# Kernel tuning notes

Hardware: AMD Instinct MI355X
Metric: run time of the kernel (lower is better)

Reference implementation:

```python
import jax, jax.numpy as jnp
import numpy as np

N = 50000
E = 1600000
IN_C = 64
HID = 16
HEADS = 4
OUT_C = 1
ATT_SLOPE = 0.2   # GATConv negative_slope for attention logits
ACT_SLOPE = 0.01  # F.leaky_relu default between layers


def _glorot(key, shape):
    fan_in, fan_out = shape[0], shape[-1]
    lim = jnp.sqrt(6.0 / (fan_in + fan_out))
    return jax.random.uniform(key, shape, jnp.float32, -lim, lim)


def setup_inputs() -> dict:
    key = jax.random.key(0)
    ks = jax.random.split(key, 12)
    x = jax.random.normal(ks[0], (N, IN_C), jnp.float32)
    edge_index = jax.random.randint(ks[1], (2, E), 0, N, jnp.int64)
    return {
        "x": x,
        "edge_index": edge_index,
        # GAT layer 1: in -> HID per head, HEADS heads (concat)
        "W1": _glorot(ks[2], (IN_C, HEADS * HID)),
        "att_src1": _glorot(ks[3], (HEADS, HID)),
        "att_dst1": _glorot(ks[4], (HEADS, HID)),
        "b1": jnp.zeros((HEADS * HID,), jnp.float32),
        # GAT layer 2: HEADS*HID -> HID, 1 head
        "W2": _glorot(ks[5], (HEADS * HID, HID)),
        "att_src2": _glorot(ks[6], (1, HID)),
        "att_dst2": _glorot(ks[7], (1, HID)),
        "b2": jnp.zeros((HID,), jnp.float32),
        # final linear
        "Wo": _glorot(ks[8], (HID, OUT_C)),
        "bo": jnp.zeros((OUT_C,), jnp.float32),
    }


def _gat_layer(x, src, dst, W, a_src, a_dst, b, n_nodes):
    """PyG GATConv (eval mode): h = xW; edge logits from additive attention;
    segment softmax over incoming edges of each dst; weighted scatter-sum."""
    H, C = a_src.shape
    h = (x @ W).reshape(n_nodes, H, C)                       # [N, H, C]
    alpha_s = jnp.einsum("nhc,hc->nh", h, a_src)             # [N, H]
    alpha_d = jnp.einsum("nhc,hc->nh", h, a_dst)             # [N, H]
    e = jax.nn.leaky_relu(alpha_s[src] + alpha_d[dst], ATT_SLOPE)  # [E, H]
    m = jax.ops.segment_max(e, dst, num_segments=n_nodes)    # [N, H]
    w = jnp.exp(e - m[dst])
    denom = jax.ops.segment_sum(w, dst, num_segments=n_nodes)
    alpha = w / denom[dst]                                   # [E, H] (self-loops => denom>0)
    out = jax.ops.segment_sum(h[src] * alpha[:, :, None], dst, num_segments=n_nodes)
    return out.reshape(n_nodes, H * C) + b                   # concat heads + bias


def reference(x, edge_index, W1, att_src1, att_dst1, b1,
              W2, att_src2, att_dst2, b2, Wo, bo):
    n = x.shape[0]
    loops = jnp.arange(n, dtype=edge_index.dtype)
    src = jnp.concatenate([edge_index[0], loops])            # add_self_loops=True
    dst = jnp.concatenate([edge_index[1], loops])
    h = _gat_layer(x, src, dst, W1, att_src1, att_dst1, b1, n)
    h = jax.nn.leaky_relu(h, ACT_SLOPE)
    h = _gat_layer(h, src, dst, W2, att_src2, att_dst2, b2, n)
    h = jax.nn.leaky_relu(h, ACT_SLOPE)
    return h @ Wo + bo                                       # [N, 1]
```

## Files before the change

### kernel.cpp

```cpp
#include <hip/hip_runtime.h>
#include <hip/hip_bf16.h>
#include <cstdint>

#define N_NODES 50000
#define N_EDGES 1600000
#define EE (N_EDGES + N_NODES)
#define BSH 7
#define BSIZE 128
#define NBUCKET ((N_NODES + BSIZE - 1) >> BSH)
#define CSH 13
#define CAP 8192
#define GEMM_BLOCKS 3125
#define BIN_BLOCKS 256

__device__ __forceinline__ float lrelu(float x, float s) { return x >= 0.f ? x : s * x; }
__device__ __forceinline__ float bflo(uint32_t v) { return __uint_as_float(v << 16); }
__device__ __forceinline__ float bfhi(uint32_t v) { return __uint_as_float(v & 0xFFFF0000u); }
__device__ __forceinline__ uint32_t bfpackhi(float a) {
    uint32_t u = __float_as_uint(a);
    u += 0x7FFF + ((u >> 16) & 1);
    return u & 0xFFFF0000u;
}
__device__ __forceinline__ uint32_t packbf(float a, float b) {
    uint32_t ua = __float_as_uint(a), ub = __float_as_uint(b);
    ua += 0x7FFF + ((ua >> 16) & 1);
    ub += 0x7FFF + ((ub >> 16) & 1);
    return (ua >> 16) | (ub & 0xFFFF0000u);
}
__device__ __forceinline__ float rdlane(float v, int l) {
    return __uint_as_float(__builtin_amdgcn_readlane(__float_as_uint(v), l));
}

__global__ __launch_bounds__(256) void k_pre(
    const float* __restrict__ x, const float* __restrict__ W1,
    const float* __restrict__ as_w, const float* __restrict__ ad_w,
    uint32_t* __restrict__ h1b, float* __restrict__ as1, float* __restrict__ ad1,
    const int* __restrict__ src, const int* __restrict__ dst,
    int* __restrict__ bcur, uint32_t* __restrict__ binned) {
    if (blockIdx.x < GEMM_BLOCKS) {
        int c = threadIdx.x & 63;
        int wv = threadIdx.x >> 6;
        float wreg[64];
#pragma unroll
        for (int k = 0; k < 64; k++) wreg[k] = W1[k * 64 + c];
        float aw = as_w[c];
        float dw = ad_w[c];
        int base = blockIdx.x * 16 + wv * 4;
#pragma unroll
        for (int r = 0; r < 4; r++) {
            int n = base + r;
            float xr = x[n * 64 + c];
            float a0 = 0.f, a1 = 0.f, a2 = 0.f, a3 = 0.f;
#pragma unroll
            for (int k = 0; k < 64; k += 4) {
                a0 = fmaf(rdlane(xr, k),     wreg[k],     a0);
                a1 = fmaf(rdlane(xr, k + 1), wreg[k + 1], a1);
                a2 = fmaf(rdlane(xr, k + 2), wreg[k + 2], a2);
                a3 = fmaf(rdlane(xr, k + 3), wreg[k + 3], a3);
            }
            float acc = (a0 + a1) + (a2 + a3);
            float other = __shfl_xor(acc, 1, 64);
            if (!(c & 1)) h1b[n * 32 + (c >> 1)] = packbf(acc, other);
            float asv = acc * aw;
            float adv = acc * dw;
#pragma unroll
            for (int off = 1; off < 16; off <<= 1) {
                asv += __shfl_xor(asv, off, 64);
                adv += __shfl_xor(adv, off, 64);
            }
            if ((c & 15) == 0) { as1[n * 4 + (c >> 4)] = asv; ad1[n * 4 + (c >> 4)] = adv; }
        }
        return;
    }
    __shared__ int lcnt[NBUCKET];
    __shared__ int lbase[NBUCKET];
    int bid = blockIdx.x - GEMM_BLOCKS;
    const int T = 16;
    const int CHUNK = 256 * T;
    int nchunks = (EE + CHUNK - 1) / CHUNK;
    for (int ch = bid; ch < nchunks; ch += BIN_BLOCKS) {
        for (int i = threadIdx.x; i < NBUCKET; i += 256) lcnt[i] = 0;
        __syncthreads();
        uint32_t pv[T];
        uint32_t pm[T];
        int base = ch * CHUNK;
#pragma unroll
        for (int k = 0; k < T; k++) {
            int e = base + k * 256 + threadIdx.x;
            if (e < EE) {
                int s, d;
                if (e < N_EDGES) { s = src[e]; d = dst[e]; } else { s = e - N_EDGES; d = s; }
                int b = d >> BSH;
                int r = atomicAdd(&lcnt[b], 1);
                pv[k] = (uint32_t)s | ((uint32_t)(d & (BSIZE - 1)) << 16);
                pm[k] = (uint32_t)r | ((uint32_t)b << 16);
            }
        }
        __syncthreads();
        for (int i = threadIdx.x; i < NBUCKET; i += 256) {
            int c = lcnt[i];
            if (c) lbase[i] = atomicAdd(&bcur[i], c);
        }
        __syncthreads();
#pragma unroll
        for (int k = 0; k < T; k++) {
            int e = base + k * 256 + threadIdx.x;
            if (e < EE) {
                int b = pm[k] >> 16, r = pm[k] & 0xFFFF;
                binned[((size_t)b << CSH) + lbase[b] + r] = pv[k];
            }
        }
        __syncthreads();
    }
}

__global__ __launch_bounds__(512) void kB_sort(const int* __restrict__ bcur, const uint32_t* __restrict__ binned,
                                               const float* __restrict__ as1, const float* __restrict__ ad1,
                                               int* __restrict__ rowdesc, uint32_t* __restrict__ sbn,
                                               uint32_t* __restrict__ wbuf) {
    int b = blockIdx.x, tid = threadIdx.x;
    int p0 = b << CSH;
    int L = bcur[b];
    __shared__ int ncnt[BSIZE];
    __shared__ int sh[BSIZE];
    __shared__ int ncur[BSIZE];
    if (tid < BSIZE) ncnt[tid] = 0;
    __syncthreads();
    for (int i = tid; i < L; i += 512) {
        uint32_t v = binned[p0 + i];
        atomicAdd(&ncnt[(v >> 16) & (BSIZE - 1)], 1);
    }
    __syncthreads();
    int v0 = 0;
    if (tid < BSIZE) { v0 = ncnt[tid]; sh[tid] = v0; }
    __syncthreads();
    for (int off = 1; off < BSIZE; off <<= 1) {
        int t = 0;
        if (tid < BSIZE && tid >= off) t = sh[tid - off];
        __syncthreads();
        if (tid < BSIZE && tid >= off) sh[tid] += t;
        __syncthreads();
    }
    if (tid < BSIZE) {
        int excl = sh[tid] - v0;
        int node = (b << BSH) + tid;
        if (node < N_NODES) rowdesc[node] = excl | (v0 << 13);
        ncur[tid] = excl;
    }
    __syncthreads();
    for (int i = tid; i < L; i += 512) {
        uint32_t v = binned[p0 + i];
        int dl = (v >> 16) & (BSIZE - 1);
        int s = (int)(v & 0xFFFF);
        int pos = atomicAdd(&ncur[dl], 1);
        int node = (b << BSH) + dl;
        float4 a = *(const float4*)(as1 + s * 4);
        float4 d = *(const float4*)(ad1 + node * 4);
        float e0 = a.x + d.x, e1 = a.y + d.y, e2 = a.z + d.z, e3 = a.w + d.w;
        float w0 = __expf(e0 >= 0.f ? e0 : 0.2f * e0);
        float w1 = __expf(e1 >= 0.f ? e1 : 0.2f * e1);
        float w2 = __expf(e2 >= 0.f ? e2 : 0.2f * e2);
        float w3 = __expf(e3 >= 0.f ? e3 : 0.2f * e3);
        sbn[p0 + pos] = (uint32_t)s | ((uint32_t)dl << 16);
        wbuf[(size_t)(p0 + pos) * 2]     = packbf(w0, w1);
        wbuf[(size_t)(p0 + pos) * 2 + 1] = packbf(w2, w3);
    }
}

__global__ __launch_bounds__(256) void k_aggr1f(
    const int* __restrict__ rowdesc, const uint32_t* __restrict__ sbn,
    const uint32_t* __restrict__ wbuf, const uint32_t* __restrict__ h1b,
    const float* __restrict__ b1, const float* __restrict__ W2,
    const float* __restrict__ as2w, const float* __restrict__ ad2w,
    float* __restrict__ h2, float* __restrict__ as2, float* __restrict__ ad2) {
    int n = blockIdx.x * 4 + (threadIdx.x >> 6);
    int lane = threadIdx.x & 63;
    int md = rowdesc[n];
    int begin = ((n >> BSH) << CSH) + (md & (CAP - 1));
    int deg = md >> 13;

    int q = lane >> 4, cl = lane & 15;
    int hc = cl >> 2;
    int wsel = hc >> 1, whalf = hc & 1;

    const uint2* h1b2 = (const uint2*)h1b;
    float acc0 = 0.f, acc1 = 0.f, acc2 = 0.f, acc3 = 0.f, dsum = 0.f;

    int iters = (deg + 3) >> 2;
#pragma unroll 4
    for (int it = 0; it < iters; it++) {
        int idx = it * 4 + q;
        uint32_t sv = sbn[begin + idx];
        uint32_t wp = wbuf[(size_t)(begin + idx) * 2 + wsel];
        float w = whalf ? bfhi(wp) : bflo(wp);
        w = (idx < deg) ? w : 0.f;
        int s = (int)(sv & 0xFFFF);
        uint2 v = h1b2[s * 16 + cl];
        dsum += w;
        acc0 += w * bflo(v.x);
        acc1 += w * bfhi(v.x);
        acc2 += w * bflo(v.y);
        acc3 += w * bfhi(v.y);
    }
#pragma unroll
    for (int off = 16; off <= 32; off <<= 1) {
        acc0 += __shfl_xor(acc0, off, 64);
        acc1 += __shfl_xor(acc1, off, 64);
        acc2 += __shfl_xor(acc2, off, 64);
        acc3 += __shfl_xor(acc3, off, 64);
        dsum += __shfl_xor(dsum, off, 64);
    }
    float dinv = 1.f / dsum;

    float4 bb = *(const float4*)(b1 + 4 * cl);
    float act0 = lrelu(acc0 * dinv + bb.x, 0.01f);
    float act1 = lrelu(acc1 * dinv + bb.y, 0.01f);
    float act2 = lrelu(acc2 * dinv + bb.z, 0.01f);
    float act3 = lrelu(acc3 * dinv + bb.w, 0.01f);

    float g = 0.f;
#pragma unroll
    for (int jj = 0; jj < 4; jj++) {
        int srcl = 4 * q + jj;
        float a0 = __shfl(act0, srcl, 64);
        float a1 = __shfl(act1, srcl, 64);
        float a2 = __shfl(act2, srcl, 64);
        float a3 = __shfl(act3, srcl, 64);
        const float* w2r = W2 + (16 * q + 4 * jj) * 16 + cl;
        g = fmaf(a0, w2r[0],  g);
        g = fmaf(a1, w2r[16], g);
        g = fmaf(a2, w2r[32], g);
        g = fmaf(a3, w2r[48], g);
    }
    g += __shfl_xor(g, 16, 64);
    g += __shfl_xor(g, 32, 64);
    if (lane < 16) h2[n * 16 + cl] = g;
    float asv = g * as2w[cl];
    float adv2 = g * ad2w[cl];
#pragma unroll
    for (int off = 1; off < 16; off <<= 1) {
        asv += __shfl_xor(asv, off, 64);
        adv2 += __shfl_xor(adv2, off, 64);
    }
    if (lane == 0) { as2[n] = asv; ad2[n] = adv2; }
}

__global__ __launch_bounds__(256) void k_w2(
    const int* __restrict__ bcur, const uint32_t* __restrict__ sbn,
    const float* __restrict__ as2, const float* __restrict__ ad2,
    uint32_t* __restrict__ earr2) {
    int slot = blockIdx.x * 256 + threadIdx.x;
    int b = slot >> CSH, i = slot & (CAP - 1);
    if (i >= bcur[b]) return;
    uint32_t v = sbn[slot];
    int s = (int)(v & 0xFFFF);
    int node = (b << BSH) + (int)(v >> 16);
    float e = as2[s] + ad2[node];
    float w = __expf(e >= 0.f ? e : 0.2f * e);
    earr2[slot] = bfpackhi(w) | (uint32_t)s;
}

__global__ __launch_bounds__(256) void k_aggr2(
    const int* __restrict__ rowdesc, const uint32_t* __restrict__ earr2,
    const float* __restrict__ h2,
    const float* __restrict__ b2, const float* __restrict__ Wo,
    const float* __restrict__ bo, float* __restrict__ out) {
    int n = blockIdx.x * 4 + (threadIdx.x >> 6);
    int lane = threadIdx.x & 63;
    int md = rowdesc[n];
    int begin = ((n >> BSH) << CSH) + (md & (CAP - 1));
    int deg = md >> 13;

    int q = lane >> 4, cl = lane & 15;
    const uint32_t* ep = earr2 + begin + q;
    float acc = 0.f, dsum = 0.f;

    int iters = (deg + 3) >> 2;
#pragma unroll 4
    for (int it = 0; it < iters; it++) {
        int idx = it * 4 + q;
        uint32_t ewd = ep[it * 4];
        float w = __uint_as_float(ewd & 0xFFFF0000u);
        w = (idx < deg) ? w : 0.f;
        int s = (int)(ewd & 0xFFFF);
        acc += w * h2[s * 16 + cl];
        dsum += w;
    }
    acc += __shfl_xor(acc, 16, 64);
    acc += __shfl_xor(acc, 32, 64);
    dsum += __shfl_xor(dsum, 16, 64);
    dsum += __shfl_xor(dsum, 32, 64);

    float val = acc / dsum + b2[cl];
    float y = lrelu(val, 0.01f) * Wo[cl];
#pragma unroll
    for (int off = 1; off < 16; off <<= 1) y += __shfl_xor(y, off, 64);
    if (lane == 0) out[n] = y + bo[0];
}

extern "C" void kernel_launch(void* const* d_in, const int* in_sizes, int n_in,
                              void* d_out, int out_size, void* d_ws, size_t ws_size,
                              hipStream_t stream) {
    const float* x    = (const float*)d_in[0];
    const int*   ei   = (const int*)d_in[1];
    const float* W1   = (const float*)d_in[2];
    const float* as1w = (const float*)d_in[3];
    const float* ad1w = (const float*)d_in[4];
    const float* b1   = (const float*)d_in[5];
    const float* W2   = (const float*)d_in[6];
    const float* as2w = (const float*)d_in[7];
    const float* ad2w = (const float*)d_in[8];
    const float* b2   = (const float*)d_in[9];
    const float* Wo   = (const float*)d_in[10];
    const float* bo   = (const float*)d_in[11];
    float* out = (float*)d_out;

    const int* srcp = ei;
    const int* dstp = ei + N_EDGES;

    char* p = (char*)d_ws;
    auto alloc = [&](size_t bytes) -> char* {
        char* r = p;
        p += (bytes + 255) / 256 * 256;
        return r;
    };
    int*      bcur    = (int*)alloc((size_t)(NBUCKET + 1) * 4);
    int*      rowdesc = (int*)alloc((size_t)N_NODES * 4);
    uint32_t* binned  = (uint32_t*)alloc((size_t)NBUCKET * CAP * 4);
    uint32_t* sbn     = (uint32_t*)alloc((size_t)NBUCKET * CAP * 4 + 256);
    uint32_t* wbuf    = (uint32_t*)alloc((size_t)NBUCKET * CAP * 8 + 256);
    uint32_t* earr2   = (uint32_t*)alloc((size_t)NBUCKET * CAP * 4 + 256);
    float*    h2      = (float*)alloc((size_t)N_NODES * 16 * 4);
    uint32_t* h1b     = (uint32_t*)alloc((size_t)N_NODES * 32 * 4);
    float*    as1     = (float*)alloc((size_t)N_NODES * 4 * 4);
    float*    ad1     = (float*)alloc((size_t)N_NODES * 4 * 4);
    float*    as2     = (float*)alloc((size_t)N_NODES * 4);
    float*    ad2     = (float*)alloc((size_t)N_NODES * 4);
    (void)alloc(2 * 1024 * 1024);

    hipMemsetAsync(bcur, 0, (size_t)(NBUCKET + 1) * 4, stream);

    k_pre<<<GEMM_BLOCKS + BIN_BLOCKS, 256, 0, stream>>>(x, W1, as1w, ad1w, h1b, as1, ad1,
                                                        srcp, dstp, bcur, binned);
    kB_sort<<<NBUCKET, 512, 0, stream>>>(bcur, binned, as1, ad1, rowdesc, sbn, wbuf);
    k_aggr1f<<<N_NODES / 4, 256, 0, stream>>>(rowdesc, sbn, wbuf, h1b, b1, W2, as2w, ad2w, h2, as2, ad2);
    k_w2<<<NBUCKET * (CAP / 256), 256, 0, stream>>>(bcur, sbn, as2, ad2, earr2);
    k_aggr2<<<N_NODES / 4, 256, 0, stream>>>(rowdesc, earr2, h2, b2, Wo, bo, out);
}
```

Baseline: 230.1 us.

## Reorder binning blocks first, single-pass sort with per-wave counts, wider aggregation gathers

The pre-kernel now launches one binning block per edge chunk (403 blocks, no grid-stride loop) ahead of the GEMM blocks, so the longer binning work starts first. The bucket sort keeps the loaded edges in registers and ranks them with per-wave shared counters. This removes the second global read and the contended atomic cursor, at the cost of a fixed 16-element-per-thread cap per bucket. Both aggregation kernels switch to 8 edge slots per wave with 128-bit and 64-bit feature gathers, for more loads in flight per node. The layer-1 W2 projection is reorganized to match.

```diff
diff --git a/kernel.cpp b/kernel.cpp
--- a/kernel.cpp
+++ b/kernel.cpp
@@ -10,8 +10,8 @@
 #define NBUCKET ((N_NODES + BSIZE - 1) >> BSH)
 #define CSH 13
 #define CAP 8192
+#define BIN_BLOCKS 403
 #define GEMM_BLOCKS 3125
-#define BIN_BLOCKS 256
 
 __device__ __forceinline__ float lrelu(float x, float s) { return x >= 0.f ? x : s * x; }
 __device__ __forceinline__ float bflo(uint32_t v) { return __uint_as_float(v << 16); }
@@ -37,53 +37,15 @@
     uint32_t* __restrict__ h1b, float* __restrict__ as1, float* __restrict__ ad1,
     const int* __restrict__ src, const int* __restrict__ dst,
     int* __restrict__ bcur, uint32_t* __restrict__ binned) {
-    if (blockIdx.x < GEMM_BLOCKS) {
-        int c = threadIdx.x & 63;
-        int wv = threadIdx.x >> 6;
-        float wreg[64];
-#pragma unroll
-        for (int k = 0; k < 64; k++) wreg[k] = W1[k * 64 + c];
-        float aw = as_w[c];
-        float dw = ad_w[c];
-        int base = blockIdx.x * 16 + wv * 4;
-#pragma unroll
-        for (int r = 0; r < 4; r++) {
-            int n = base + r;
-            float xr = x[n * 64 + c];
-            float a0 = 0.f, a1 = 0.f, a2 = 0.f, a3 = 0.f;
-#pragma unroll
-            for (int k = 0; k < 64; k += 4) {
-                a0 = fmaf(rdlane(xr, k),     wreg[k],     a0);
-                a1 = fmaf(rdlane(xr, k + 1), wreg[k + 1], a1);
-                a2 = fmaf(rdlane(xr, k + 2), wreg[k + 2], a2);
-                a3 = fmaf(rdlane(xr, k + 3), wreg[k + 3], a3);
-            }
-            float acc = (a0 + a1) + (a2 + a3);
-            float other = __shfl_xor(acc, 1, 64);
-            if (!(c & 1)) h1b[n * 32 + (c >> 1)] = packbf(acc, other);
-            float asv = acc * aw;
-            float adv = acc * dw;
-#pragma unroll
-            for (int off = 1; off < 16; off <<= 1) {
-                asv += __shfl_xor(asv, off, 64);
-                adv += __shfl_xor(adv, off, 64);
-            }
-            if ((c & 15) == 0) { as1[n * 4 + (c >> 4)] = asv; ad1[n * 4 + (c >> 4)] = adv; }
-        }
-        return;
-    }
-    __shared__ int lcnt[NBUCKET];
-    __shared__ int lbase[NBUCKET];
-    int bid = blockIdx.x - GEMM_BLOCKS;
-    const int T = 16;
-    const int CHUNK = 256 * T;
-    int nchunks = (EE + CHUNK - 1) / CHUNK;
-    for (int ch = bid; ch < nchunks; ch += BIN_BLOCKS) {
+    if (blockIdx.x < BIN_BLOCKS) {
+        __shared__ int lcnt[NBUCKET];
+        __shared__ int lbase[NBUCKET];
+        const int T = 16;
         for (int i = threadIdx.x; i < NBUCKET; i += 256) lcnt[i] = 0;
         __syncthreads();
         uint32_t pv[T];
         uint32_t pm[T];
-        int base = ch * CHUNK;
+        int base = blockIdx.x * (256 * T);
 #pragma unroll
         for (int k = 0; k < T; k++) {
             int e = base + k * 256 + threadIdx.x;
@@ -110,7 +72,39 @@
                 binned[((size_t)b << CSH) + lbase[b] + r] = pv[k];
             }
         }
-        __syncthreads();
+        return;
+    }
+    int c = threadIdx.x & 63;
+    int wv = threadIdx.x >> 6;
+    float wreg[64];
+#pragma unroll
+    for (int k = 0; k < 64; k++) wreg[k] = W1[k * 64 + c];
+    float aw = as_w[c];
+    float dw = ad_w[c];
+    int base = (blockIdx.x - BIN_BLOCKS) * 16 + wv * 4;
+#pragma unroll
+    for (int r = 0; r < 4; r++) {
+        int n = base + r;
+        float xr = x[n * 64 + c];
+        float a0 = 0.f, a1 = 0.f, a2 = 0.f, a3 = 0.f;
+#pragma unroll
+        for (int k = 0; k < 64; k += 4) {
+            a0 = fmaf(rdlane(xr, k),     wreg[k],     a0);
+            a1 = fmaf(rdlane(xr, k + 1), wreg[k + 1], a1);
+            a2 = fmaf(rdlane(xr, k + 2), wreg[k + 2], a2);
+            a3 = fmaf(rdlane(xr, k + 3), wreg[k + 3], a3);
+        }
+        float acc = (a0 + a1) + (a2 + a3);
+        float other = __shfl_xor(acc, 1, 64);
+        if (!(c & 1)) h1b[n * 32 + (c >> 1)] = packbf(acc, other);
+        float asv = acc * aw;
+        float adv = acc * dw;
+#pragma unroll
+        for (int off = 1; off < 16; off <<= 1) {
+            asv += __shfl_xor(asv, off, 64);
+            adv += __shfl_xor(adv, off, 64);
+        }
+        if ((c & 15) == 0) { as1[n * 4 + (c >> 4)] = asv; ad1[n * 4 + (c >> 4)] = adv; }
     }
 }
 
@@ -118,52 +112,72 @@
                                                const float* __restrict__ as1, const float* __restrict__ ad1,
                                                int* __restrict__ rowdesc, uint32_t* __restrict__ sbn,
                                                uint32_t* __restrict__ wbuf) {
-    int b = blockIdx.x, tid = threadIdx.x;
+    int b = blockIdx.x, tid = threadIdx.x, wv = tid >> 6;
     int p0 = b << CSH;
     int L = bcur[b];
-    __shared__ int ncnt[BSIZE];
-    __shared__ int sh[BSIZE];
-    __shared__ int ncur[BSIZE];
-    if (tid < BSIZE) ncnt[tid] = 0;
+    __shared__ int cnt8[8][BSIZE];
+    __shared__ int wbase[8][BSIZE];
+    __shared__ int shs[BSIZE];
+    for (int i = tid; i < 8 * BSIZE; i += 512) ((int*)cnt8)[i] = 0;
     __syncthreads();
-    for (int i = tid; i < L; i += 512) {
-        uint32_t v = binned[p0 + i];
-        atomicAdd(&ncnt[(v >> 16) & (BSIZE - 1)], 1);
+
+    uint32_t pv[16];
+    unsigned short rk[16];
+#pragma unroll
+    for (int k = 0; k < 16; k++) {
+        int i = tid + k * 512;
+        if (i < L) {
+            uint32_t v = binned[p0 + i];
+            pv[k] = v;
+            rk[k] = (unsigned short)atomicAdd(&cnt8[wv][(v >> 16) & (BSIZE - 1)], 1);
+        }
     }
     __syncthreads();
-    int v0 = 0;
-    if (tid < BSIZE) { v0 = ncnt[tid]; sh[tid] = v0; }
+
+    int tot = 0;
+    if (tid < BSIZE) {
+#pragma unroll
+        for (int w = 0; w < 8; w++) tot += cnt8[w][tid];
+        shs[tid] = tot;
+    }
     __syncthreads();
     for (int off = 1; off < BSIZE; off <<= 1) {
         int t = 0;
-        if (tid < BSIZE && tid >= off) t = sh[tid - off];
-        __syncthreads();
-        if (tid < BSIZE && tid >= off) sh[tid] += t;
+        if (tid < BSIZE && tid >= off) t = shs[tid - off];
+        __syncthreads();
+        if (tid < BSIZE && tid >= off) shs[tid] += t;
         __syncthreads();
     }
     if (tid < BSIZE) {
-        int excl = sh[tid] - v0;
+        int excl = shs[tid] - tot;
         int node = (b << BSH) + tid;
-        if (node < N_NODES) rowdesc[node] = excl | (v0 << 13);
-        ncur[tid] = excl;
+        if (node < N_NODES) rowdesc[node] = excl | (tot << 13);
+        int wb = excl;
+#pragma unroll
+        for (int w = 0; w < 8; w++) { wbase[w][tid] = wb; wb += cnt8[w][tid]; }
     }
     __syncthreads();
-    for (int i = tid; i < L; i += 512) {
-        uint32_t v = binned[p0 + i];
-        int dl = (v >> 16) & (BSIZE - 1);
-        int s = (int)(v & 0xFFFF);
-        int pos = atomicAdd(&ncur[dl], 1);
-        int node = (b << BSH) + dl;
-        float4 a = *(const float4*)(as1 + s * 4);
-        float4 d = *(const float4*)(ad1 + node * 4);
-        float e0 = a.x + d.x, e1 = a.y + d.y, e2 = a.z + d.z, e3 = a.w + d.w;
-        float w0 = __expf(e0 >= 0.f ? e0 : 0.2f * e0);
-        float w1 = __expf(e1 >= 0.f ? e1 : 0.2f * e1);
-        float w2 = __expf(e2 >= 0.f ? e2 : 0.2f * e2);
-        float w3 = __expf(e3 >= 0.f ? e3 : 0.2f * e3);
-        sbn[p0 + pos] = (uint32_t)s | ((uint32_t)dl << 16);
-        wbuf[(size_t)(p0 + pos) * 2]     = packbf(w0, w1);
-        wbuf[(size_t)(p0 + pos) * 2 + 1] = packbf(w2, w3);
+
+#pragma unroll
+    for (int k = 0; k < 16; k++) {
+        int i = tid + k * 512;
+        if (i < L) {
+            uint32_t v = pv[k];
+            int dl = (v >> 16) & (BSIZE - 1);
+            int s = (int)(v & 0xFFFF);
+            int pos = wbase[wv][dl] + (int)rk[k];
+            int node = (b << BSH) + dl;
+            float4 a = *(const float4*)(as1 + s * 4);
+            float4 d = *(const float4*)(ad1 + node * 4);
+            float e0 = a.x + d.x, e1 = a.y + d.y, e2 = a.z + d.z, e3 = a.w + d.w;
+            float w0 = __expf(e0 >= 0.f ? e0 : 0.2f * e0);
+            float w1 = __expf(e1 >= 0.f ? e1 : 0.2f * e1);
+            float w2 = __expf(e2 >= 0.f ? e2 : 0.2f * e2);
+            float w3 = __expf(e3 >= 0.f ? e3 : 0.2f * e3);
+            sbn[p0 + pos] = (uint32_t)s | ((uint32_t)dl << 16);
+            wbuf[(size_t)(p0 + pos) * 2]     = packbf(w0, w1);
+            wbuf[(size_t)(p0 + pos) * 2 + 1] = packbf(w2, w3);
+        }
     }
 }
 
@@ -179,64 +193,75 @@
     int begin = ((n >> BSH) << CSH) + (md & (CAP - 1));
     int deg = md >> 13;
 
-    int q = lane >> 4, cl = lane & 15;
-    int hc = cl >> 2;
+    int slot = lane >> 3, cl = lane & 7;
+    int hc = cl >> 1;
     int wsel = hc >> 1, whalf = hc & 1;
 
-    const uint2* h1b2 = (const uint2*)h1b;
-    float acc0 = 0.f, acc1 = 0.f, acc2 = 0.f, acc3 = 0.f, dsum = 0.f;
-
-    int iters = (deg + 3) >> 2;
+    const uint4* h1b4 = (const uint4*)h1b;
+    float a0 = 0.f, a1 = 0.f, a2 = 0.f, a3 = 0.f, a4 = 0.f, a5 = 0.f, a6 = 0.f, a7 = 0.f, dsum = 0.f;
+
+    int iters = (deg + 7) >> 3;
 #pragma unroll 4
     for (int it = 0; it < iters; it++) {
-        int idx = it * 4 + q;
+        int idx = it * 8 + slot;
         uint32_t sv = sbn[begin + idx];
         uint32_t wp = wbuf[(size_t)(begin + idx) * 2 + wsel];
         float w = whalf ? bfhi(wp) : bflo(wp);
         w = (idx < deg) ? w : 0.f;
         int s = (int)(sv & 0xFFFF);
-        uint2 v = h1b2[s * 16 + cl];
+        uint4 v = h1b4[s * 8 + cl];
         dsum += w;
-        acc0 += w * bflo(v.x);
-        acc1 += w * bfhi(v.x);
-        acc2 += w * bflo(v.y);
-        acc3 += w * bfhi(v.y);
-    }
-#pragma unroll
-    for (int off = 16; off <= 32; off <<= 1) {
-        acc0 += __shfl_xor(acc0, off, 64);
-        acc1 += __shfl_xor(acc1, off, 64);
-        acc2 += __shfl_xor(acc2, off, 64);
-        acc3 += __shfl_xor(acc3, off, 64);
+        a0 += w * bflo(v.x); a1 += w * bfhi(v.x);
+        a2 += w * bflo(v.y); a3 += w * bfhi(v.y);
+        a4 += w * bflo(v.z); a5 += w * bfhi(v.z);
+        a6 += w * bflo(v.w); a7 += w * bfhi(v.w);
+    }
+#pragma unroll
+    for (int off = 8; off <= 32; off <<= 1) {
+        a0 += __shfl_xor(a0, off, 64); a1 += __shfl_xor(a1, off, 64);
+        a2 += __shfl_xor(a2, off, 64); a3 += __shfl_xor(a3, off, 64);
+        a4 += __shfl_xor(a4, off, 64); a5 += __shfl_xor(a5, off, 64);
+        a6 += __shfl_xor(a6, off, 64); a7 += __shfl_xor(a7, off, 64);
         dsum += __shfl_xor(dsum, off, 64);
     }
     float dinv = 1.f / dsum;
 
-    float4 bb = *(const float4*)(b1 + 4 * cl);
-    float act0 = lrelu(acc0 * dinv + bb.x, 0.01f);
-    float act1 = lrelu(acc1 * dinv + bb.y, 0.01f);
-    float act2 = lrelu(acc2 * dinv + bb.z, 0.01f);
-    float act3 = lrelu(acc3 * dinv + bb.w, 0.01f);
-
+    float4 bb0 = *(const float4*)(b1 + 8 * cl);
+    float4 bb1 = *(const float4*)(b1 + 8 * cl + 4);
+    float act0 = lrelu(a0 * dinv + bb0.x, 0.01f);
+    float act1 = lrelu(a1 * dinv + bb0.y, 0.01f);
+    float act2 = lrelu(a2 * dinv + bb0.z, 0.01f);
+    float act3 = lrelu(a3 * dinv + bb0.w, 0.01f);
+    float act4 = lrelu(a4 * dinv + bb1.x, 0.01f);
+    float act5 = lrelu(a5 * dinv + bb1.y, 0.01f);
+    float act6 = lrelu(a6 * dinv + bb1.z, 0.01f);
+    float act7 = lrelu(a7 * dinv + bb1.w, 0.01f);
+
+    int co = lane & 15, kg = lane >> 4;
+    int l0 = 2 * kg, l1 = 2 * kg + 1;
+    const float* w2r = W2 + (16 * kg) * 16 + co;
     float g = 0.f;
-#pragma unroll
-    for (int jj = 0; jj < 4; jj++) {
-        int srcl = 4 * q + jj;
-        float a0 = __shfl(act0, srcl, 64);
-        float a1 = __shfl(act1, srcl, 64);
-        float a2 = __shfl(act2, srcl, 64);
-        float a3 = __shfl(act3, srcl, 64);
-        const float* w2r = W2 + (16 * q + 4 * jj) * 16 + cl;
-        g = fmaf(a0, w2r[0],  g);
-        g = fmaf(a1, w2r[16], g);
-        g = fmaf(a2, w2r[32], g);
-        g = fmaf(a3, w2r[48], g);
-    }
+    g = fmaf(__shfl(act0, l0, 64), w2r[0 * 16],  g);
+    g = fmaf(__shfl(act1, l0, 64), w2r[1 * 16],  g);
+    g = fmaf(__shfl(act2, l0, 64), w2r[2 * 16],  g);
+    g = fmaf(__shfl(act3, l0, 64), w2r[3 * 16],  g);
+    g = fmaf(__shfl(act4, l0, 64), w2r[4 * 16],  g);
+    g = fmaf(__shfl(act5, l0, 64), w2r[5 * 16],  g);
+    g = fmaf(__shfl(act6, l0, 64), w2r[6 * 16],  g);
+    g = fmaf(__shfl(act7, l0, 64), w2r[7 * 16],  g);
+    g = fmaf(__shfl(act0, l1, 64), w2r[8 * 16],  g);
+    g = fmaf(__shfl(act1, l1, 64), w2r[9 * 16],  g);
+    g = fmaf(__shfl(act2, l1, 64), w2r[10 * 16], g);
+    g = fmaf(__shfl(act3, l1, 64), w2r[11 * 16], g);
+    g = fmaf(__shfl(act4, l1, 64), w2r[12 * 16], g);
+    g = fmaf(__shfl(act5, l1, 64), w2r[13 * 16], g);
+    g = fmaf(__shfl(act6, l1, 64), w2r[14 * 16], g);
+    g = fmaf(__shfl(act7, l1, 64), w2r[15 * 16], g);
     g += __shfl_xor(g, 16, 64);
     g += __shfl_xor(g, 32, 64);
-    if (lane < 16) h2[n * 16 + cl] = g;
-    float asv = g * as2w[cl];
-    float adv2 = g * ad2w[cl];
+    if (lane < 16) h2[n * 16 + co] = g;
+    float asv = g * as2w[co];
+    float adv2 = g * ad2w[co];
 #pragma unroll
     for (int off = 1; off < 16; off <<= 1) {
         asv += __shfl_xor(asv, off, 64);
@@ -271,30 +296,35 @@
     int begin = ((n >> BSH) << CSH) + (md & (CAP - 1));
     int deg = md >> 13;
 
-    int q = lane >> 4, cl = lane & 15;
-    const uint32_t* ep = earr2 + begin + q;
-    float acc = 0.f, dsum = 0.f;
-
-    int iters = (deg + 3) >> 2;
+    int slot = lane >> 3, c2 = lane & 7;
+    const float2* h22 = (const float2*)h2;
+    float acc0 = 0.f, acc1 = 0.f, dsum = 0.f;
+
+    int iters = (deg + 7) >> 3;
 #pragma unroll 4
     for (int it = 0; it < iters; it++) {
-        int idx = it * 4 + q;
-        uint32_t ewd = ep[it * 4];
+        int idx = it * 8 + slot;
+        uint32_t ewd = earr2[begin + idx];
         float w = __uint_as_float(ewd & 0xFFFF0000u);
         w = (idx < deg) ? w : 0.f;
         int s = (int)(ewd & 0xFFFF);
-        acc += w * h2[s * 16 + cl];
+        float2 hv = h22[s * 8 + c2];
+        acc0 += w * hv.x;
+        acc1 += w * hv.y;
         dsum += w;
     }
-    acc += __shfl_xor(acc, 16, 64);
-    acc += __shfl_xor(acc, 32, 64);
-    dsum += __shfl_xor(dsum, 16, 64);
-    dsum += __shfl_xor(dsum, 32, 64);
-
-    float val = acc / dsum + b2[cl];
-    float y = lrelu(val, 0.01f) * Wo[cl];
-#pragma unroll
-    for (int off = 1; off < 16; off <<= 1) y += __shfl_xor(y, off, 64);
+#pragma unroll
+    for (int off = 8; off <= 32; off <<= 1) {
+        acc0 += __shfl_xor(acc0, off, 64);
+        acc1 += __shfl_xor(acc1, off, 64);
+        dsum += __shfl_xor(dsum, off, 64);
+    }
+    float v0 = lrelu(acc0 / dsum + b2[2 * c2], 0.01f) * Wo[2 * c2];
+    float v1 = lrelu(acc1 / dsum + b2[2 * c2 + 1], 0.01f) * Wo[2 * c2 + 1];
+    float y = v0 + v1;
+    y += __shfl_xor(y, 1, 64);
+    y += __shfl_xor(y, 2, 64);
+    y += __shfl_xor(y, 4, 64);
     if (lane == 0) out[n] = y + bo[0];
 }
 
@@ -336,11 +366,11 @@
     float*    ad1     = (float*)alloc((size_t)N_NODES * 4 * 4);
     float*    as2     = (float*)alloc((size_t)N_NODES * 4);
     float*    ad2     = (float*)alloc((size_t)N_NODES * 4);
-    (void)alloc(2 * 1024 * 1024);
+    (void)alloc(3 * 1024 * 1024);
 
     hipMemsetAsync(bcur, 0, (size_t)(NBUCKET + 1) * 4, stream);
 
-    k_pre<<<GEMM_BLOCKS + BIN_BLOCKS, 256, 0, stream>>>(x, W1, as1w, ad1w, h1b, as1, ad1,
+    k_pre<<<BIN_BLOCKS + GEMM_BLOCKS, 256, 0, stream>>>(x, W1, as1w, ad1w, h1b, as1, ad1,
                                                         srcp, dstp, bcur, binned);
     kB_sort<<<NBUCKET, 512, 0, stream>>>(bcur, binned, as1, ad1, rowdesc, sbn, wbuf);
     k_aggr1f<<<N_NODES / 4, 256, 0, stream>>>(rowdesc, sbn, wbuf, h1b, b1, W2, as2w, ad2w, h2, as2, ad2);
```

Result: faster. 218.9 us (-4.9%).
